# Kernel tuning notes

Measured on AMD Instinct MI355X. Metric: run time of the kernel, lower is better.

The kernel has to match this reference:

```python
import jax, jax.numpy as jnp
import numpy as np

EMBEDDING_SIZE = 50
MAX_DOCUMENT_LENGTH = 100
MAX_LABEL = 15
VOCAB = 200000
HID = 1024
BATCH = 4096


def setup_inputs() -> dict:
    key = jax.random.key(0)
    ks = jax.random.split(key, 8)
    x = jax.random.randint(ks[0], (BATCH, MAX_DOCUMENT_LENGTH), 0, VOCAB)
    emb_table = jax.random.normal(ks[1], (VOCAB, EMBEDDING_SIZE), jnp.float32) * 0.05
    # Keras GRUCell (reset_after=True): kernel [E,3H], recurrent_kernel [H,3H],
    # bias [2,3H] split into input bias and recurrent bias; gate order z, r, h.
    kernel = jax.random.normal(ks[2], (EMBEDDING_SIZE, 3 * HID), jnp.float32) * (1.0 / np.sqrt(EMBEDDING_SIZE))
    rec_kernel = jax.random.normal(ks[3], (HID, 3 * HID), jnp.float32) * (1.0 / np.sqrt(HID))
    bias_i = jnp.zeros((3 * HID,), jnp.float32)
    bias_r = jnp.zeros((3 * HID,), jnp.float32)
    Wd = jax.random.normal(ks[4], (HID, MAX_LABEL), jnp.float32) * (1.0 / np.sqrt(HID))
    bd = jnp.zeros((MAX_LABEL,), jnp.float32)
    return {"x": x, "drop_rate": 0, "emb_table": emb_table, "kernel": kernel,
            "rec_kernel": rec_kernel, "bias_i": bias_i, "bias_r": bias_r,
            "Wd": Wd, "bd": bd}


def _gru_scan(emb, kernel, rec_kernel, bias_i, bias_r):
    # emb: [B,T,E] -> time-major [T,B,E]
    emb_t = jnp.transpose(emb, (1, 0, 2))
    B = emb.shape[0]
    h0 = jnp.zeros((B, HID), emb.dtype)

    def step(h, x_t):
        xp = x_t @ kernel + bias_i            # [B,3H]
        hp = h @ rec_kernel + bias_r          # [B,3H]
        xz, xr, xh = jnp.split(xp, 3, axis=-1)
        hz, hr, hh = jnp.split(hp, 3, axis=-1)
        z = jax.nn.sigmoid(xz + hz)
        r = jax.nn.sigmoid(xr + hr)
        hcand = jnp.tanh(xh + r * hh)
        h_new = z * h + (1.0 - z) * hcand
        return h_new, None

    h_last, _ = jax.lax.scan(step, h0, emb_t)
    return h_last


def reference(x, drop_rate, emb_table, kernel, rec_kernel, bias_i, bias_r, Wd, bd):
    emb = emb_table[x]                         # [B,T,E]
    encoding = _gru_scan(emb, kernel, rec_kernel, bias_i, bias_r)  # [B,H]
    if drop_rate > 0:                          # drop_rate is a static Python int
        keep = 1.0 - float(drop_rate)
        mask = jax.random.bernoulli(jax.random.key(1), keep, encoding.shape)
        encoding = jnp.where(mask, encoding / keep, 0.0)
    logits = encoding @ Wd + bd                # [B,15]
    return logits
```

## Files before the change

kernel.cpp:

```cpp
#include <hip/hip_runtime.h>
#include <stdint.h>

#define H_DIM   1024
#define G3      3072
#define EMB     50
#define TSTEPS  100
#define NB      4096
#define NLABEL  15

typedef __bf16 bf16x8 __attribute__((ext_vector_type(8)));
typedef float  f32x4  __attribute__((ext_vector_type(4)));
typedef int    i32x4  __attribute__((ext_vector_type(4)));

__device__ inline uint16_t f2bf(float f) {
  uint32_t u = __builtin_bit_cast(uint32_t, f);
  u += 0x7FFFu + ((u >> 16) & 1u);
  return (uint16_t)(u >> 16);
}

__device__ inline void gld16(const void* g, void* l) {
  __builtin_amdgcn_global_load_lds(
      (const __attribute__((address_space(1))) uint32_t*)g,
      (__attribute__((address_space(3))) uint32_t*)l, 16, 0, 0);
}

#define VM(n) do { asm volatile("s_waitcnt vmcnt(" #n ")" ::: "memory"); \
                   __builtin_amdgcn_sched_barrier(0); } while (0)
#define LGKM0() do { asm volatile("s_waitcnt lgkmcnt(0)" ::: "memory"); \
                     __builtin_amdgcn_sched_barrier(0); } while (0)
#define BARF() do { __builtin_amdgcn_s_barrier(); \
                    asm volatile("" ::: "memory"); } while (0)


__global__ __launch_bounds__(256) void prep_recT(const float* __restrict__ rec,
                                                 uint16_t* __restrict__ recT) {
  __shared__ uint16_t st[64][72];
  const int n0 = blockIdx.x * 64;
  const int k0 = blockIdx.y * 64;
  const int tid = threadIdx.x;
#pragma unroll
  for (int i = 0; i < 16; ++i) {
    int idx = tid + i * 256;
    int r = idx >> 6;
    int c = idx & 63;
    st[c][r] = f2bf(rec[(size_t)(k0 + r) * G3 + n0 + c]);
  }
  __syncthreads();
#pragma unroll
  for (int i = 0; i < 16; ++i) {
    int idx = tid + i * 256;
    int r = idx >> 6;
    int c = idx & 63;
    recT[(size_t)(n0 + r) * H_DIM + k0 + c] = st[r][c];
  }
}

__global__ __launch_bounds__(256) void prep_kerT(const float* __restrict__ ker,
                                                 uint16_t* __restrict__ kerT) {
  int n = blockIdx.x * 4 + (threadIdx.x >> 6);
  int k = threadIdx.x & 63;
  float v = (k < EMB) ? ker[(size_t)k * G3 + n] : 0.f;
  kerT[(size_t)n * 64 + k] = f2bf(v);
}

__global__ __launch_bounds__(256) void prep_pack(const uint16_t* __restrict__ recT,
                                                 const uint16_t* __restrict__ kerT,
                                                 uint16_t* __restrict__ Bpk) {
  int cid = blockIdx.x * 256 + threadIdx.x;
  int lane = cid & 63;
  int r = cid >> 6;
  int ks = r & 1; r >>= 1;
  int nf = r & 1; r >>= 1;
  int wn = r & 1; r >>= 1;
  int g  = r % 3; r /= 3;
  int kt = r % 17;
  int colblk = r / 17;
  int n  = g * H_DIM + colblk * 64 + wn * 32 + nf * 16 + (lane & 15);
  int kk = ks * 32 + (lane >> 4) * 8;
  const uint16_t* src = (kt < 16) ? recT + (size_t)n * H_DIM + kt * 64 + kk
                                  : kerT + (size_t)n * 64 + kk;
  *reinterpret_cast<i32x4*>(Bpk + (size_t)cid * 8) =
      *reinterpret_cast<const i32x4*>(src);
}

__global__ __launch_bounds__(256) void prep_embt(const int* __restrict__ x,
                                                 const float* __restrict__ tab,
                                                 uint16_t* __restrict__ embt) {
  int idx = blockIdx.x * 256 + threadIdx.x;
  int g = idx >> 5;
  int p = idx & 31;
  int t = g >> 12;
  int b = g & 4095;
  int row = x[b * TSTEPS + t];
  float2 v;
  if (p < 25) v = *reinterpret_cast<const float2*>(tab + (size_t)row * EMB + 2 * p);
  else { v.x = 0.f; v.y = 0.f; }
  uint32_t packed = (uint32_t)f2bf(v.x) | ((uint32_t)f2bf(v.y) << 16);
  *reinterpret_cast<uint32_t*>(embt + (size_t)g * 64 + 2 * p) = packed;
}

__global__ __launch_bounds__(256, 2) void gru_step_kernel(
    const uint16_t* __restrict__ hb_prev,
    float* __restrict__ hf,
    uint16_t* __restrict__ hb_next,
    const uint16_t* __restrict__ Bpk,
    const uint16_t* __restrict__ embt,
    const float* __restrict__ bias_i,
    const float* __restrict__ bias_r) {
  __shared__ __align__(16) uint16_t sA2[2][128 * 64];
  __shared__ __align__(16) uint16_t sB2[2][12288];

  const int tid  = threadIdx.x;
  const int lane = tid & 63;
  const int wid  = tid >> 6;
  const int wm   = wid >> 1;
  const int wn   = wid & 1;
  const int bid  = blockIdx.x;
  const int xk = bid & 7, slot = bid >> 3;
  const int rowblk = (xk >> 1) * 8 + (slot >> 3);
  const int colblk = (xk & 1) * 8 + (slot & 7);
  const int r0 = rowblk * 128;
  const int j0 = colblk * 64;

  const int swz8 = 8 * ((lane & 7) ^ (lane >> 3));

  const uint16_t* pBcol = Bpk + (size_t)colblk * 17 * 12288;

  bf16x8 af[4][2];
  bf16x8 bfr[3][2][2];
  f32x4 accZ[4][2], accR[4][2], accH[4][2], accX[4][2];
#pragma unroll
  for (int m = 0; m < 4; ++m)
#pragma unroll
    for (int n = 0; n < 2; ++n) {
      accZ[m][n] = (f32x4){0.f, 0.f, 0.f, 0.f};
      accR[m][n] = (f32x4){0.f, 0.f, 0.f, 0.f};
      accH[m][n] = (f32x4){0.f, 0.f, 0.f, 0.f};
      accX[m][n] = (f32x4){0.f, 0.f, 0.f, 0.f};
    }

  auto stageA = [&](int t) {
    const int abuf = t & 1;
#pragma unroll
    for (int i = 0; i < 4; ++i) {
      int chunk = wid * 4 + i;
      int row = chunk * 8 + (lane >> 3);
      const uint16_t* src = (t < 16)
          ? hb_prev + (size_t)(r0 + row) * H_DIM + t * 64 + swz8
          : embt + (size_t)(r0 + row) * 64 + swz8;
      gld16(src, &sA2[abuf][(chunk * 64 + lane) * 8]);
    }
  };
  auto stageB = [&](int t) {
    const int bbuf = t & 1;
    const uint16_t* base = pBcol + (size_t)t * 12288;
#pragma unroll
    for (int i = 0; i < 6; ++i) {
      int e = (i * 256 + tid) * 8;
      gld16(base + e, &sB2[bbuf][e]);
    }
  };
  auto readA = [&](int t) {
    const int abuf = t & 1;
#pragma unroll
    for (int ks = 0; ks < 2; ++ks) {
      const int colswz = (ks * 32 + (lane >> 4) * 8) ^ ((lane & 7) << 3);
#pragma unroll
      for (int mf = 0; mf < 4; ++mf)
        af[mf][ks] = *reinterpret_cast<const bf16x8*>(
            &sA2[abuf][(wm * 64 + mf * 16 + (lane & 15)) * 64 + colswz]);
    }
  };
  auto readB = [&](int t) {
    const int bbuf = t & 1;
#pragma unroll
    for (int g = 0; g < 3; ++g)
#pragma unroll
      for (int nf = 0; nf < 2; ++nf)
#pragma unroll
        for (int ks = 0; ks < 2; ++ks) {
          int c = g * 8 + wn * 4 + nf * 2 + ks;
          bfr[g][nf][ks] = *reinterpret_cast<const bf16x8*>(
              &sB2[bbuf][c * 512 + lane * 8]);
        }
  };

#define MFG(g, ACC) do { \
    __builtin_amdgcn_s_setprio(1); \
    _Pragma("unroll") for (int ks = 0; ks < 2; ++ks) \
    _Pragma("unroll") for (int nf = 0; nf < 2; ++nf) \
    _Pragma("unroll") for (int mf = 0; mf < 4; ++mf) \
      ACC[mf][nf] = __builtin_amdgcn_mfma_f32_16x16x32_bf16( \
          af[mf][ks], bfr[g][nf][ks], ACC[mf][nf], 0, 0, 0); \
    __builtin_amdgcn_s_setprio(0); \
  } while (0)

  stageA(0); stageB(0);
  stageA(1); stageB(1);
  VM(10);
  BARF();
  readA(0); readB(0);
  LGKM0();

  for (int t = 0; t < 15; ++t) {
    BARF();
    stageA(t + 2); stageB(t + 2);
    MFG(0, accZ);
    MFG(1, accR);
    MFG(2, accH);
    VM(10);
    BARF();
    readA(t + 1); readB(t + 1);
    LGKM0();
  }

  MFG(0, accZ);
  MFG(1, accR);
  MFG(2, accH);
  VM(0);
  BARF();
  readA(16); readB(16);
  LGKM0();
  MFG(0, accZ);
  MFG(1, accR);
  MFG(2, accX);

#undef MFG

#pragma unroll
  for (int nf = 0; nf < 2; ++nf) {
    int col = j0 + wn * 32 + nf * 16 + (lane & 15);
    float b_z = bias_i[col] + bias_r[col];
    float b_r = bias_i[H_DIM + col] + bias_r[H_DIM + col];
    float bih = bias_i[2 * H_DIM + col];
    float brh = bias_r[2 * H_DIM + col];
#pragma unroll
    for (int mf = 0; mf < 4; ++mf) {
#pragma unroll
      for (int q = 0; q < 4; ++q) {
        int row = r0 + wm * 64 + mf * 16 + (lane >> 4) * 4 + q;
        float z  = 1.f / (1.f + __expf(-(accZ[mf][nf][q] + b_z)));
        float rr = 1.f / (1.f + __expf(-(accR[mf][nf][q] + b_r)));
        float pre = accX[mf][nf][q] + bih + rr * (accH[mf][nf][q] + brh);
        float hc  = 2.f / (1.f + __expf(-2.f * pre)) - 1.f;
        size_t idx = (size_t)row * H_DIM + col;
        float hold = hf[idx];
        float hnew = z * hold + (1.f - z) * hc;
        hf[idx] = hnew;
        hb_next[idx] = f2bf(hnew);
      }
    }
  }
}

__global__ __launch_bounds__(64) void logits_kernel(const float* __restrict__ hf,
                                                    const float* __restrict__ Wd,
                                                    const float* __restrict__ bd,
                                                    float* __restrict__ out) {
  int b = blockIdx.x;
  int l = threadIdx.x;
  float p[NLABEL];
#pragma unroll
  for (int o = 0; o < NLABEL; ++o) p[o] = 0.f;
  for (int kb = 0; kb < 16; ++kb) {
    int k = kb * 64 + l;
    float hv = hf[(size_t)b * H_DIM + k];
#pragma unroll
    for (int o = 0; o < NLABEL; ++o) p[o] += hv * Wd[k * NLABEL + o];
  }
#pragma unroll
  for (int o = 0; o < NLABEL; ++o) {
#pragma unroll
    for (int s = 32; s; s >>= 1) p[o] += __shfl_xor(p[o], s);
  }
  if (l == 0) {
#pragma unroll
    for (int o = 0; o < NLABEL; ++o) out[(size_t)b * NLABEL + o] = p[o] + bd[o];
  }
}

extern "C" void kernel_launch(void* const* d_in, const int* in_sizes, int n_in,
                              void* d_out, int out_size, void* d_ws, size_t ws_size,
                              hipStream_t stream) {
  const int*   x          = (const int*)d_in[0];
  const float* emb_table  = (const float*)d_in[2];
  const float* kernel_w   = (const float*)d_in[3];
  const float* rec_kernel = (const float*)d_in[4];
  const float* bias_i     = (const float*)d_in[5];
  const float* bias_r     = (const float*)d_in[6];
  const float* Wd         = (const float*)d_in[7];
  const float* bd         = (const float*)d_in[8];
  float* out = (float*)d_out;

  char* ws = (char*)d_ws;
  size_t off = 0;
  auto alloc = [&](size_t bytes) {
    char* p = ws + off;
    off += (bytes + 255) & ~(size_t)255;
    return p;
  };
  float*    hf   = (float*)alloc((size_t)NB * H_DIM * 4);
  uint16_t* hb0  = (uint16_t*)alloc((size_t)NB * H_DIM * 2);
  uint16_t* hb1  = (uint16_t*)alloc((size_t)NB * H_DIM * 2);
  uint16_t* recT = (uint16_t*)alloc((size_t)G3 * H_DIM * 2);
  uint16_t* kerT = (uint16_t*)alloc((size_t)G3 * 64 * 2);
  uint16_t* embt = (uint16_t*)alloc((size_t)TSTEPS * NB * 64 * 2);
  uint16_t* Bpk  = (uint16_t*)alloc((size_t)16 * 17 * 12288 * 2);
  if (off > ws_size) return;

  hipMemsetAsync(hf, 0, (size_t)NB * H_DIM * 4, stream);
  hipMemsetAsync(hb0, 0, (size_t)NB * H_DIM * 2, stream);

  prep_recT<<<dim3(G3 / 64, H_DIM / 64), 256, 0, stream>>>(rec_kernel, recT);
  prep_kerT<<<G3 / 4, 256, 0, stream>>>(kernel_w, kerT);
  prep_pack<<<1632, 256, 0, stream>>>(recT, kerT, Bpk);
  prep_embt<<<TSTEPS * NB * 32 / 256, 256, 0, stream>>>(x, emb_table, embt);

  uint16_t* hb[2] = {hb0, hb1};
  for (int t = 0; t < TSTEPS; ++t) {
    gru_step_kernel<<<512, 256, 0, stream>>>(
        hb[t & 1], hf, hb[(t + 1) & 1], Bpk,
        embt + (size_t)t * NB * 64, bias_i, bias_r);
  }
  logits_kernel<<<NB, 64, 0, stream>>>(hf, Wd, bd, out);
}
```

Before: 3.134 ms.

## Split GRU step block across 8 waves with smaller per-wave tiles

Doubles the threads per block from 256 to 512 and rearranges the 8 waves as a 2x4 grid, so each wave computes a 64x16 output tile per gate instead of 64x32. The global-to-LDS staging loops are halved per thread and the vmcnt waits are adjusted to match. Per-wave registers (accumulators and B fragments) drop, with the aim of more waves per CU for latency hiding. In exchange each wave reuses its A fragments over fewer MFMAs and more LDS reads are issued per MFMA.

```diff
diff --git a/kernel.cpp b/kernel.cpp
--- a/kernel.cpp
+++ b/kernel.cpp
@@ -99,7 +99,7 @@
   *reinterpret_cast<uint32_t*>(embt + (size_t)g * 64 + 2 * p) = packed;
 }
 
-__global__ __launch_bounds__(256, 2) void gru_step_kernel(
+__global__ __launch_bounds__(512, 4) void gru_step_kernel(
     const uint16_t* __restrict__ hb_prev,
     float* __restrict__ hf,
     uint16_t* __restrict__ hb_next,
@@ -113,8 +113,8 @@
   const int tid  = threadIdx.x;
   const int lane = tid & 63;
   const int wid  = tid >> 6;
-  const int wm   = wid >> 1;
-  const int wn   = wid & 1;
+  const int wm   = wid >> 2;
+  const int wn   = wid & 3;
   const int bid  = blockIdx.x;
   const int xk = bid & 7, slot = bid >> 3;
   const int rowblk = (xk >> 1) * 8 + (slot >> 3);
@@ -127,23 +127,21 @@
   const uint16_t* pBcol = Bpk + (size_t)colblk * 17 * 12288;
 
   bf16x8 af[4][2];
-  bf16x8 bfr[3][2][2];
-  f32x4 accZ[4][2], accR[4][2], accH[4][2], accX[4][2];
-#pragma unroll
-  for (int m = 0; m < 4; ++m)
-#pragma unroll
-    for (int n = 0; n < 2; ++n) {
-      accZ[m][n] = (f32x4){0.f, 0.f, 0.f, 0.f};
-      accR[m][n] = (f32x4){0.f, 0.f, 0.f, 0.f};
-      accH[m][n] = (f32x4){0.f, 0.f, 0.f, 0.f};
-      accX[m][n] = (f32x4){0.f, 0.f, 0.f, 0.f};
-    }
+  bf16x8 bfr[3][2];
+  f32x4 accZ[4], accR[4], accH[4], accX[4];
+#pragma unroll
+  for (int m = 0; m < 4; ++m) {
+    accZ[m] = (f32x4){0.f, 0.f, 0.f, 0.f};
+    accR[m] = (f32x4){0.f, 0.f, 0.f, 0.f};
+    accH[m] = (f32x4){0.f, 0.f, 0.f, 0.f};
+    accX[m] = (f32x4){0.f, 0.f, 0.f, 0.f};
+  }
 
   auto stageA = [&](int t) {
     const int abuf = t & 1;
 #pragma unroll
-    for (int i = 0; i < 4; ++i) {
-      int chunk = wid * 4 + i;
+    for (int i = 0; i < 2; ++i) {
+      int chunk = wid * 2 + i;
       int row = chunk * 8 + (lane >> 3);
       const uint16_t* src = (t < 16)
           ? hb_prev + (size_t)(r0 + row) * H_DIM + t * 64 + swz8
@@ -155,8 +153,8 @@
     const int bbuf = t & 1;
     const uint16_t* base = pBcol + (size_t)t * 12288;
 #pragma unroll
-    for (int i = 0; i < 6; ++i) {
-      int e = (i * 256 + tid) * 8;
+    for (int i = 0; i < 3; ++i) {
+      int e = (i * 512 + tid) * 8;
       gld16(base + e, &sB2[bbuf][e]);
     }
   };
@@ -176,28 +174,25 @@
 #pragma unroll
     for (int g = 0; g < 3; ++g)
 #pragma unroll
-      for (int nf = 0; nf < 2; ++nf)
-#pragma unroll
-        for (int ks = 0; ks < 2; ++ks) {
-          int c = g * 8 + wn * 4 + nf * 2 + ks;
-          bfr[g][nf][ks] = *reinterpret_cast<const bf16x8*>(
-              &sB2[bbuf][c * 512 + lane * 8]);
-        }
+      for (int ks = 0; ks < 2; ++ks) {
+        int c = g * 8 + wn * 2 + ks;
+        bfr[g][ks] = *reinterpret_cast<const bf16x8*>(
+            &sB2[bbuf][c * 512 + lane * 8]);
+      }
   };
 
 #define MFG(g, ACC) do { \
     __builtin_amdgcn_s_setprio(1); \
     _Pragma("unroll") for (int ks = 0; ks < 2; ++ks) \
-    _Pragma("unroll") for (int nf = 0; nf < 2; ++nf) \
     _Pragma("unroll") for (int mf = 0; mf < 4; ++mf) \
-      ACC[mf][nf] = __builtin_amdgcn_mfma_f32_16x16x32_bf16( \
-          af[mf][ks], bfr[g][nf][ks], ACC[mf][nf], 0, 0, 0); \
+      ACC[mf] = __builtin_amdgcn_mfma_f32_16x16x32_bf16( \
+          af[mf][ks], bfr[g][ks], ACC[mf], 0, 0, 0); \
     __builtin_amdgcn_s_setprio(0); \
   } while (0)
 
   stageA(0); stageB(0);
   stageA(1); stageB(1);
-  VM(10);
+  VM(5);
   BARF();
   readA(0); readB(0);
   LGKM0();
@@ -208,7 +203,7 @@
     MFG(0, accZ);
     MFG(1, accR);
     MFG(2, accH);
-    VM(10);
+    VM(5);
     BARF();
     readA(t + 1); readB(t + 1);
     LGKM0();
@@ -227,21 +222,20 @@
 
 #undef MFG
 
-#pragma unroll
-  for (int nf = 0; nf < 2; ++nf) {
-    int col = j0 + wn * 32 + nf * 16 + (lane & 15);
-    float b_z = bias_i[col] + bias_r[col];
-    float b_r = bias_i[H_DIM + col] + bias_r[H_DIM + col];
-    float bih = bias_i[2 * H_DIM + col];
-    float brh = bias_r[2 * H_DIM + col];
+  {
+    const int col = j0 + wn * 16 + (lane & 15);
+    const float b_z = bias_i[col] + bias_r[col];
+    const float b_r = bias_i[H_DIM + col] + bias_r[H_DIM + col];
+    const float bih = bias_i[2 * H_DIM + col];
+    const float brh = bias_r[2 * H_DIM + col];
 #pragma unroll
     for (int mf = 0; mf < 4; ++mf) {
 #pragma unroll
       for (int q = 0; q < 4; ++q) {
         int row = r0 + wm * 64 + mf * 16 + (lane >> 4) * 4 + q;
-        float z  = 1.f / (1.f + __expf(-(accZ[mf][nf][q] + b_z)));
-        float rr = 1.f / (1.f + __expf(-(accR[mf][nf][q] + b_r)));
-        float pre = accX[mf][nf][q] + bih + rr * (accH[mf][nf][q] + brh);
+        float z  = 1.f / (1.f + __expf(-(accZ[mf][q] + b_z)));
+        float rr = 1.f / (1.f + __expf(-(accR[mf][q] + b_r)));
+        float pre = accX[mf][q] + bih + rr * (accH[mf][q] + brh);
         float hc  = 2.f / (1.f + __expf(-2.f * pre)) - 1.f;
         size_t idx = (size_t)row * H_DIM + col;
         float hold = hf[idx];
@@ -318,7 +312,7 @@
 
   uint16_t* hb[2] = {hb0, hb1};
   for (int t = 0; t < TSTEPS; ++t) {
-    gru_step_kernel<<<512, 256, 0, stream>>>(
+    gru_step_kernel<<<512, 512, 0, stream>>>(
         hb[t & 1], hf, hb[(t + 1) & 1], Bpk,
         embt + (size_t)t * NB * 64, bias_i, bias_r);
   }
```

Result: faster. 3.035 ms (median of 2 runs) (-3.1%).
